# Optimization experiments

Measured on AMD Instinct MI355X. Metric: run time of the kernel, lower is better.

Reference implementation:

```python
import jax, jax.numpy as jnp
import numpy as np

N, L, H, D = 4, 1024, 8, 64

def setup_inputs() -> dict:
    key = jax.random.key(0)
    ks = jax.random.split(key, 6)
    names = ["q_real", "q_imag", "k_real", "k_imag", "v_real", "v_imag"]
    return {n: jax.random.normal(k, (N, L, H, D), dtype=jnp.float32) for n, k in zip(names, ks)}


def reference(q_real, q_imag, k_real, k_imag, v_real, v_imag):
    d = q_real.shape[-1]
    scale = 1.0 / np.sqrt(d).astype(np.float32)
    # complex QK^T: (ar+i*ai)(br+i*bi) -> 4 real einsums, scores shape (N,H,L,S)
    s_real = (jnp.einsum('nlhd,nshd->nhls', q_real, k_real)
              - jnp.einsum('nlhd,nshd->nhls', q_imag, k_imag))
    s_imag = (jnp.einsum('nlhd,nshd->nhls', q_real, k_imag)
              + jnp.einsum('nlhd,nshd->nhls', q_imag, k_real))
    # complex softmax = independent softmax on real and imag parts
    w_real = jax.nn.softmax(scale * s_real, axis=-1)
    w_imag = jax.nn.softmax(scale * s_imag, axis=-1)
    # complex_dropout on complex input is identity (original code drops nothing)
    # complex AV
    u_real = (jnp.einsum('nhls,nshd->nlhd', w_real, v_real)
              - jnp.einsum('nhls,nshd->nlhd', w_imag, v_imag))
    u_imag = (jnp.einsum('nhls,nshd->nlhd', w_real, v_imag)
              + jnp.einsum('nhls,nshd->nlhd', w_imag, v_real))
    # attn_weights.permute(0,2,1,3).mean(dim=-2): (N,H,L,S)->(N,L,H,S), mean over H -> (N,L,S)
    a_real = w_real.mean(axis=1)
    a_imag = w_imag.mean(axis=1)
    return (u_real, u_imag, a_real, a_imag)
```

## Files before the change

kernel.cpp:

```cpp
#include <hip/hip_runtime.h>

#define N_ 4
#define L_ 1024
#define H_ 8
#define D_ 64

typedef _Float16 f16x8 __attribute__((ext_vector_type(8)));
typedef _Float16 f16x4 __attribute__((ext_vector_type(4)));
typedef _Float16 f16x2 __attribute__((ext_vector_type(2)));
typedef float f32x4 __attribute__((ext_vector_type(4)));

#define MFMA(A, B, C) __builtin_amdgcn_mfma_f32_16x16x32_f16(A, B, C, 0, 0, 0)
#define EXP2(x) __builtin_amdgcn_exp2f(x)

__device__ __forceinline__ ushort f2h(float x) {
    union { _Float16 h; ushort u; } c;
    c.h = (_Float16)x;
    return c.u;
}
__device__ __forceinline__ f16x8 ld8(const ushort* p) {
    return *(const f16x8*)p;
}
__device__ __forceinline__ f16x4 pack4(float a, float b, float c, float d) {
    union { f16x4 v; f16x2 h[2]; } u;
    u.h[0] = __builtin_bit_cast(f16x2, __builtin_amdgcn_cvt_pkrtz(a, b));
    u.h[1] = __builtin_bit_cast(f16x2, __builtin_amdgcn_cvt_pkrtz(c, d));
    return u.v;
}
__device__ __forceinline__ f16x8 negf(f16x8 a) {
    uint4 u = __builtin_bit_cast(uint4, a);
    u.x ^= 0x80008000u; u.y ^= 0x80008000u; u.z ^= 0x80008000u; u.w ^= 0x80008000u;
    return __builtin_bit_cast(f16x8, u);
}
__device__ __forceinline__ f16x8 cvt8s(const float* p, float s) {
    float4 a = *(const float4*)p;
    float4 b = *(const float4*)(p + 4);
    union { f16x8 v; _Float16 e[8]; } u;
    u.e[0] = (_Float16)(a.x * s); u.e[1] = (_Float16)(a.y * s);
    u.e[2] = (_Float16)(a.z * s); u.e[3] = (_Float16)(a.w * s);
    u.e[4] = (_Float16)(b.x * s); u.e[5] = (_Float16)(b.y * s);
    u.e[6] = (_Float16)(b.z * s); u.e[7] = (_Float16)(b.w * s);
    return u.v;
}
#define SCQ 0.18033688011112f
__device__ __forceinline__ f16x8 cvt8(const float* p) { return cvt8s(p, SCQ); }

__device__ __forceinline__ void gl_lds16(const ushort* g, ushort* l) {
    __builtin_amdgcn_global_load_lds(
        (const __attribute__((address_space(1))) unsigned int*)g,
        (__attribute__((address_space(3))) unsigned int*)l, 16, 0, 0);
}

__global__ void cvt_k(const float* __restrict__ k_r, const float* __restrict__ k_i,
                      ushort* __restrict__ dst) {
    int gid = blockIdx.x * 256 + threadIdx.x;
    int aid = gid >> 19;
    int idx = (gid & 0x7FFFF) << 2;
    int d  = idx & 63;
    int l  = (idx >> 6) & 1023;
    int hh = (idx >> 16) & 7;
    int n  = idx >> 19;
    const float* src = aid ? k_i : k_r;
    const float4 v = *(const float4*)(src + (((long)n * 1024 + l) * 8 + hh) * 64 + d);
    ushort4 o = make_ushort4(f2h(v.x), f2h(v.y), f2h(v.z), f2h(v.w));
    *(ushort4*)(dst + ((long)aid << 21) + idx) = o;
}

__global__ void cvt_v(const float* __restrict__ vr, const float* __restrict__ vi,
                      ushort* __restrict__ dst) {
    __shared__ ushort t[64][72];
    int bid = blockIdx.x;
    int aid = bid >> 9;
    int b   = bid & 511;
    int s0  = (b & 15) << 6;
    int hh  = (b >> 4) & 7;
    int n   = b >> 7;
    const float* src = aid ? vi : vr;
    int tid = threadIdx.x;
    int r  = tid >> 4;
    int cq = (tid & 15) << 2;
#pragma unroll
    for (int it = 0; it < 4; ++it) {
        int s = s0 + it * 16 + r;
        const float4 v = *(const float4*)(src + (((long)n * 1024 + s) * 8 + hh) * 64 + cq);
        t[it * 16 + r][cq + 0] = f2h(v.x);
        t[it * 16 + r][cq + 1] = f2h(v.y);
        t[it * 16 + r][cq + 2] = f2h(v.z);
        t[it * 16 + r][cq + 3] = f2h(v.w);
    }
    __syncthreads();
    const int rem = cq & 31;
    const int noff = (cq & 32) + (((rem & 15) >> 2) << 3) + ((rem >> 4) << 2);
#pragma unroll
    for (int it = 0; it < 4; ++it) {
        int dd = it * 16 + r;
        ushort4 o;
        o.x = t[cq + 0][dd]; o.y = t[cq + 1][dd]; o.z = t[cq + 2][dd]; o.w = t[cq + 3][dd];
        *(ushort4*)(dst + ((long)aid << 21) + (((long)n * 8 + hh) * 64 + dd) * 1024 + s0 + noff) = o;
    }
}


__launch_bounds__(512, 4)
__global__ void attn_u(const float* __restrict__ qr_g, const float* __restrict__ qi_g,
                       const ushort* __restrict__ ws, float* __restrict__ rdbuf,
                       float* __restrict__ out) {
    __shared__ ushort stgK[2][4096];
    __shared__ ushort stgV[2][4096];

    const int tid  = threadIdx.x;
    const int lane = tid & 63;
    const int wv   = tid >> 6;
    const int p    = wv >> 2;
    const int lsub = wv & 3;
    const int col  = lane & 15;
    const int g    = lane >> 4;

    const int id = blockIdx.x;
    const int x  = id & 7;
    const int j  = id >> 3;
    const int nh = x * 4 + (j >> 4);
    const int n  = nh >> 3;
    const int h  = nh & 7;
    const int l0 = (j & 15) * 64 + lsub * 16;

    const ushort* Kr = ws + ((long)nh << 16);
    const ushort* Ki = ws + (1l << 21) + ((long)nh << 16);
    const ushort* Vr = ws + (2l << 21) + ((long)nh << 16);
    const ushort* Vi = ws + (3l << 21) + ((long)nh << 16);

    const long qg = (((long)n * 1024 + l0 + col) * 8 + h) * 64 + g * 8;
    const float sgn = p ? SCQ : -SCQ;
    const f16x8 qr0 = cvt8(qr_g + qg), qr1 = cvt8(qr_g + qg + 32);
    const f16x8 qx0 = cvt8s(qi_g + qg, sgn), qx1 = cvt8s(qi_g + qg + 32, sgn);

    const int kpart = tid >> 8;
    const int ksr   = (tid >> 3) & 31;
    const int kbo   = (tid & 7) ^ (ksr & 7);
    const ushort* Ksrc = (kpart ? Ki : Kr);
    const int vd  = tid >> 3;
    const int vb  = (tid & 7) ^ (vd & 7);
    const ushort* Vsrc = ((vb >> 2) ? Vi : Vr);
    const int vbo = (vb & 3) * 8;
    ushort* kdst0 = &stgK[0][wv * 512];
    ushort* kdst1 = &stgK[1][wv * 512];
    ushort* vdst0 = &stgV[0][wv * 512];
    ushort* vdst1 = &stgV[1][wv * 512];

    float dsum = 0.f;
    f32x4 uA[4], uB[4];
#pragma unroll
    for (int db = 0; db < 4; ++db) {
        uA[db] = (f32x4){0.f, 0.f, 0.f, 0.f};
        uB[db] = (f32x4){0.f, 0.f, 0.f, 0.f};
    }

    const int kx  = (g ^ (col & 7)) * 8;
    const int kx2 = ((g + 4) ^ (col & 7)) * 8;
    const int vxA = (g ^ (col & 7)) * 8;
    const int vxB = ((4 + g) ^ (col & 7)) * 8;

#define STAGE(kd, vd_, cc)                                                   \
    do {                                                                     \
        gl_lds16(Ksrc + (long)((cc) * 32 + ksr) * 64 + kbo * 8, kd);         \
        gl_lds16(Vsrc + (long)vd * 1024 + (cc) * 32 + vbo, vd_);             \
    } while (0)

    STAGE(kdst0, vdst0, 0);
    __syncthreads();

    for (int cc = 0; cc < 32; ++cc) {
        const int buf = cc & 1;
        if (cc < 31) {
            if (buf) STAGE(kdst0, vdst0, cc + 1);
            else     STAGE(kdst1, vdst1, cc + 1);
        }
        const ushort* sk = stgK[buf];
        const ushort* sv = stgV[buf];

        union { f16x8 w8; f16x4 q[2]; } pw;
#pragma unroll
        for (int sb = 0; sb < 2; ++sb) {
            const int rb = (sb * 16 + col) * 64;
            f16x8 ka0 = ld8(&sk[p * 2048 + rb + kx]);
            f16x8 ka1 = ld8(&sk[p * 2048 + rb + kx2]);
            f16x8 kb0 = ld8(&sk[(p ^ 1) * 2048 + rb + kx]);
            f16x8 kb1 = ld8(&sk[(p ^ 1) * 2048 + rb + kx2]);
            f32x4 a0 = (f32x4){0.f, 0.f, 0.f, 0.f};
            a0 = MFMA(ka0, qr0, a0); a0 = MFMA(ka1, qr1, a0);
            a0 = MFMA(kb0, qx0, a0); a0 = MFMA(kb1, qx1, a0);
            const float w0 = EXP2(a0[0]), w1 = EXP2(a0[1]);
            const float w2 = EXP2(a0[2]), w3 = EXP2(a0[3]);
            dsum += (w0 + w1) + (w2 + w3);
            pw.q[sb] = pack4(w0, w1, w2, w3);
        }

        __builtin_amdgcn_s_setprio(1);
#pragma unroll
        for (int db = 0; db < 4; ++db) {
            const int rv = (db * 16 + col) * 64;
            uA[db] = MFMA(pw.w8, ld8(&sv[rv + vxA]), uA[db]);
            uB[db] = MFMA(pw.w8, ld8(&sv[rv + vxB]), uB[db]);
        }
        __builtin_amdgcn_s_setprio(0);

        __syncthreads();
    }

    dsum += __shfl_xor(dsum, 16);
    dsum += __shfl_xor(dsum, 32);
    const float rd = 1.f / dsum;
    if (lane < 16) rdbuf[p * 32768 + nh * 1024 + l0 + col] = rd;

    float rdl[4];
#pragma unroll
    for (int r = 0; r < 4; ++r) rdl[r] = __shfl(rd, 4 * g + r);

#pragma unroll
    for (int db = 0; db < 4; ++db) {
#pragma unroll
        for (int r = 0; r < 4; ++r) {
            uA[db][r] *= rdl[r];
            uB[db][r] *= rdl[r];
        }
    }

    float* cb = (float*)&stgK[0][0];
    const int ci = (lsub * 64 + lane) * 16;
    if (p == 1) {
#pragma unroll
        for (int db = 0; db < 4; ++db) *(f32x4*)&cb[ci + db * 4] = uB[db];
    }
    __syncthreads();
    f32x4 oR[4];
    if (p == 0) {
#pragma unroll
        for (int db = 0; db < 4; ++db) oR[db] = uA[db] - *(f32x4*)&cb[ci + db * 4];
    }
    __syncthreads();
    if (p == 1) {
#pragma unroll
        for (int db = 0; db < 4; ++db) *(f32x4*)&cb[ci + db * 4] = uA[db];
    }
    __syncthreads();

    if (p == 0) {
        const long OFF_UI = 2097152;
#pragma unroll
        for (int db = 0; db < 4; ++db) {
            f32x4 oI = uB[db] + *(f32x4*)&cb[ci + db * 4];
#pragma unroll
            for (int r = 0; r < 4; ++r) {
                const int l = l0 + 4 * g + r;
                const int d = db * 16 + col;
                const long base = (((long)n * L_ + l) * H_ + h) * D_ + d;
                out[base] = oR[db][r];
                out[OFF_UI + base] = oI[r];
            }
        }
    }
#undef STAGE
}

__launch_bounds__(256, 4)
__global__ void kern_a(const float* __restrict__ qr_g, const float* __restrict__ qi_g,
                      const ushort* __restrict__ ws, const float* __restrict__ rdbuf,
                      float* __restrict__ out) {
    __shared__ ushort stgK[2][2][64][64];
    __shared__ float lrd[8][2][64];

    const int tid  = threadIdx.x;
    const int lane = tid & 63;
    const int wv   = tid >> 6;
    const int col  = lane & 15;
    const int g    = lane >> 4;

    const int id  = blockIdx.x;
    const int x   = id & 7;
    const int q   = id >> 3;
    const int n   = x >> 1;
    const int idx = (x & 1) * 128 + q;
    const int lt0 = (idx >> 4) * 64;
    const int sc  = idx & 15;
    const int l0  = lt0 + wv * 16;

    const ushort* KrB = ws + ((long)(n * 8) << 16);
    const ushort* KiB = ws + (1l << 21) + ((long)(n * 8) << 16);

#pragma unroll
    for (int i = 0; i < 4; ++i) {
        const int t = i * 256 + tid;
        (&lrd[0][0][0])[t] =
            rdbuf[((t >> 6) & 1) * 32768 + (n * 8 + (t >> 7)) * 1024 + lt0 + (t & 63)];
    }

    const int sp   = wv >> 1;
    const int kbs  = ((lane & 7) ^ (lane >> 3)) * 8;

#define STAGEA(buf, hh)                                                      \
    do {                                                                     \
        const ushort* Kp = (sp ? KiB : KrB) + ((long)(hh) << 16);            \
        _Pragma("unroll")                                                    \
        for (int i = 0; i < 4; ++i) {                                        \
            const int krow = (wv & 1) * 32 + i * 8 + (lane >> 3);            \
            gl_lds16(Kp + (long)(sc * 64 + krow) * 64 + kbs,                 \
                     &stgK[buf][sp][(wv & 1) * 32 + i * 8][0]);              \
        }                                                                    \
    } while (0)

    f32x4 aR[4], aI[4];
#pragma unroll
    for (int i = 0; i < 4; ++i) {
        aR[i] = (f32x4){0.f, 0.f, 0.f, 0.f};
        aI[i] = (f32x4){0.f, 0.f, 0.f, 0.f};
    }

    const int kx  = (g ^ (col & 7)) * 8;
    const int kx2 = ((g + 4) ^ (col & 7)) * 8;

    STAGEA(0, 0);
    __syncthreads();

    for (int h = 0; h < 8; ++h) {
        const int buf = h & 1;
        if (h < 7) STAGEA(buf ^ 1, h + 1);

        const long qg = (((long)n * 1024 + l0 + col) * 8 + h) * 64 + g * 8;
        const f16x8 qr0 = cvt8(qr_g + qg), qr1 = cvt8(qr_g + qg + 32);
        const f16x8 qi0 = cvt8(qi_g + qg), qi1 = cvt8(qi_g + qg + 32);
        const f16x8 qn0 = negf(qi0), qn1 = negf(qi1);

        float rdR[4], rdI[4];
#pragma unroll
        for (int r = 0; r < 4; ++r) {
            rdR[r] = lrd[h][0][wv * 16 + 4 * g + r];
            rdI[r] = lrd[h][1][wv * 16 + 4 * g + r];
        }

#pragma unroll
        for (int sb = 0; sb < 4; ++sb) {
            const int row = sb * 16 + col;
            f16x8 kr0 = ld8(&stgK[buf][0][row][kx]);
            f16x8 kr1 = ld8(&stgK[buf][0][row][kx2]);
            f16x8 ki0 = ld8(&stgK[buf][1][row][kx]);
            f16x8 ki1 = ld8(&stgK[buf][1][row][kx2]);
            f32x4 a0 = (f32x4){0.f, 0.f, 0.f, 0.f};
            a0 = MFMA(qr0, kr0, a0); a0 = MFMA(qr1, kr1, a0);
            a0 = MFMA(qn0, ki0, a0); a0 = MFMA(qn1, ki1, a0);
            f32x4 a1 = (f32x4){0.f, 0.f, 0.f, 0.f};
            a1 = MFMA(qr0, ki0, a1); a1 = MFMA(qr1, ki1, a1);
            a1 = MFMA(qi0, kr0, a1); a1 = MFMA(qi1, kr1, a1);
#pragma unroll
            for (int r = 0; r < 4; ++r) {
                aR[sb][r] += EXP2(a0[r]) * rdR[r];
                aI[sb][r] += EXP2(a1[r]) * rdI[r];
            }
        }
        __syncthreads();
    }

    const long OFF_AR = 4194304;
    const long OFF_AI = 8388608;
#pragma unroll
    for (int sb = 0; sb < 4; ++sb) {
#pragma unroll
        for (int r = 0; r < 4; ++r) {
            const int l = l0 + 4 * g + r;
            const int s = sc * 64 + sb * 16 + col;
            const long ab = ((long)n * 1024 + l) * 1024 + s;
            out[OFF_AR + ab] = aR[sb][r] * 0.125f;
            out[OFF_AI + ab] = aI[sb][r] * 0.125f;
        }
    }
#undef STAGEA
}

extern "C" void kernel_launch(void* const* d_in, const int* in_sizes, int n_in,
                              void* d_out, int out_size, void* d_ws, size_t ws_size,
                              hipStream_t stream) {
    const float* qr = (const float*)d_in[0];
    const float* qi = (const float*)d_in[1];
    const float* kr = (const float*)d_in[2];
    const float* ki = (const float*)d_in[3];
    const float* vr = (const float*)d_in[4];
    const float* vi = (const float*)d_in[5];
    ushort* ws = (ushort*)d_ws;
    float* rdbuf = (float*)((char*)d_ws + (16ull << 20));
    float* out = (float*)d_out;

    hipLaunchKernelGGL(cvt_k, dim3(4096), dim3(256), 0, stream, kr, ki, ws);
    hipLaunchKernelGGL(cvt_v, dim3(1024), dim3(256), 0, stream, vr, vi, ws + (2l << 21));
    hipLaunchKernelGGL(attn_u, dim3(512), dim3(512), 0, stream, qr, qi, ws, rdbuf, out);
    hipLaunchKernelGGL(kern_a, dim3(1024), dim3(256), 0, stream, qr, qi, ws, rdbuf, out);
}
```

Baseline: 96.48 us.

## Triple-buffer K/V staging with explicit vmcnt waits in attn_u loop

Grows the LDS staging for K and V from two buffers to three and keeps two chunks of async global-to-LDS loads in flight. Each iteration now waits with s_waitcnt vmcnt(2) plus a raw s_barrier instead of a full __syncthreads. This hides more global-load latency behind the MFMA work. It costs more LDS per block (48KB vs 32KB), which may cut occupancy under launch_bounds(512,4), and a __syncthreads is added before the epilogue reuses stgK.

```diff
diff --git a/kernel.cpp b/kernel.cpp
--- a/kernel.cpp
+++ b/kernel.cpp
@@ -105,8 +105,8 @@
 __global__ void attn_u(const float* __restrict__ qr_g, const float* __restrict__ qi_g,
                        const ushort* __restrict__ ws, float* __restrict__ rdbuf,
                        float* __restrict__ out) {
-    __shared__ ushort stgK[2][4096];
-    __shared__ ushort stgV[2][4096];
+    __shared__ ushort stgK[3][4096];
+    __shared__ ushort stgV[3][4096];
 
     const int tid  = threadIdx.x;
     const int lane = tid & 63;
@@ -142,10 +142,8 @@
     const int vb  = (tid & 7) ^ (vd & 7);
     const ushort* Vsrc = ((vb >> 2) ? Vi : Vr);
     const int vbo = (vb & 3) * 8;
-    ushort* kdst0 = &stgK[0][wv * 512];
-    ushort* kdst1 = &stgK[1][wv * 512];
-    ushort* vdst0 = &stgV[0][wv * 512];
-    ushort* vdst1 = &stgV[1][wv * 512];
+    ushort* kbase = &stgK[0][0] + wv * 512;
+    ushort* vbase = &stgV[0][0] + wv * 512;
 
     float dsum = 0.f;
     f32x4 uA[4], uB[4];
@@ -160,23 +158,27 @@
     const int vxA = (g ^ (col & 7)) * 8;
     const int vxB = ((4 + g) ^ (col & 7)) * 8;
 
-#define STAGE(kd, vd_, cc)                                                   \
+#define STAGE(bb, cc)                                                        \
     do {                                                                     \
-        gl_lds16(Ksrc + (long)((cc) * 32 + ksr) * 64 + kbo * 8, kd);         \
-        gl_lds16(Vsrc + (long)vd * 1024 + (cc) * 32 + vbo, vd_);             \
+        gl_lds16(Ksrc + (long)((cc) * 32 + ksr) * 64 + kbo * 8,              \
+                 kbase + (bb) * 4096);                                       \
+        gl_lds16(Vsrc + (long)vd * 1024 + (cc) * 32 + vbo,                   \
+                 vbase + (bb) * 4096);                                       \
     } while (0)
 
-    STAGE(kdst0, vdst0, 0);
-    __syncthreads();
-
+    STAGE(0, 0);
+    STAGE(1, 1);
+    asm volatile("s_waitcnt vmcnt(2)" ::: "memory");
+    __builtin_amdgcn_s_barrier();
+
+    int bc = 0;
     for (int cc = 0; cc < 32; ++cc) {
-        const int buf = cc & 1;
-        if (cc < 31) {
-            if (buf) STAGE(kdst0, vdst0, cc + 1);
-            else     STAGE(kdst1, vdst1, cc + 1);
-        }
-        const ushort* sk = stgK[buf];
-        const ushort* sv = stgV[buf];
+        if (cc < 30) {
+            const int bp = (cc + 2 >= 3) ? (cc + 2) % 3 : cc + 2;
+            STAGE(bp, cc + 2);
+        }
+        const ushort* sk = &stgK[0][0] + bc * 4096;
+        const ushort* sv = &stgV[0][0] + bc * 4096;
 
         union { f16x8 w8; f16x4 q[2]; } pw;
 #pragma unroll
@@ -204,7 +206,12 @@
         }
         __builtin_amdgcn_s_setprio(0);
 
-        __syncthreads();
+        if (cc < 31) {
+            if (cc < 30) asm volatile("s_waitcnt vmcnt(2)" ::: "memory");
+            else         asm volatile("s_waitcnt vmcnt(0)" ::: "memory");
+            __builtin_amdgcn_s_barrier();
+        }
+        bc = (bc == 2) ? 0 : bc + 1;
     }
 
     dsum += __shfl_xor(dsum, 16);
@@ -225,6 +232,7 @@
         }
     }
 
+    __syncthreads();
     float* cb = (float*)&stgK[0][0];
     const int ci = (lsub * 64 + lane) * 16;
     if (p == 1) {
```

Result: slower. 99.36 us (+3.0%).
